# Performance work log

Hardware: AMD Instinct MI355X
Metric: run time of the kernel (lower is better)

Reference implementation:

```python
import jax, jax.numpy as jnp
import numpy as np

TEMP = 0.05
MOMENTUM = 0.2
EPS = 1e-12
B, D, N = 256, 2048, 30000


def setup_inputs() -> dict:
    key = jax.random.key(0)
    k1, k2, k3 = jax.random.split(key, 3)
    inputs = jax.random.normal(k1, (B, D), dtype=jnp.float32)
    feats = jax.random.normal(k2, (N, D), dtype=jnp.float32)
    # cluster memory bank rows are unit-normalized in practice
    feats = feats / (jnp.linalg.norm(feats, axis=1, keepdims=True) + EPS)
    targets = jax.random.randint(k3, (B,), 0, N, dtype=jnp.int64)
    return {"inputs": inputs, "features": feats, "targets": targets}


def reference(inputs, features, targets):
    # F.normalize(inputs, dim=1)
    x = inputs / (jnp.linalg.norm(inputs, axis=1, keepdims=True) + EPS)
    # outputs = x @ features.T / temp  -> [B, N]
    logits = jnp.einsum("bd,nd->bn", x, features) / TEMP
    # loss = F.cross_entropy(outputs, targets)
    logp = jax.nn.log_softmax(logits, axis=1)
    loss = -jnp.mean(jnp.take_along_axis(logp, targets[:, None], axis=1))

    # CM backward side effect: sequential per-sample momentum update + renorm of bank.
    # features[y] = m*features[y] + (1-m)*x ; features[y] /= ||features[y]||
    def step(bank, xy):
        xi, yi = xy
        f = MOMENTUM * bank[yi] + (1.0 - MOMENTUM) * xi
        f = f / (jnp.linalg.norm(f) + EPS)
        return bank.at[yi].set(f), None

    new_features, _ = jax.lax.scan(step, features, (x, targets))
    return loss, new_features
```

## Files before the change

kernel.cpp:

```cpp
#include <hip/hip_runtime.h>
#include <hip/hip_bf16.h>

#define B_ 256
#define D_ 2048
#define N_ 30000
#define INV_TEMP 20.0f
#define MOM 0.2f
#define EPSF 1e-12f
#define BN 48
#define KC 64
#define KH 1024
#define NKH 16
#define NT 625
#define NBL 40
#define TPB 16

typedef __attribute__((ext_vector_type(8))) short bf16x8;
typedef __attribute__((ext_vector_type(4))) float f32x4;

typedef const __attribute__((address_space(1))) void* gas_t;
typedef __attribute__((address_space(3))) void* las_t;
#define GLOAD16(g, l) __builtin_amdgcn_global_load_lds((gas_t)(g), (las_t)(l), 16, 0, 0)

__device__ __forceinline__ unsigned short f2bf(float f) {
  union { float f; unsigned int u; } v; v.f = f;
  unsigned int u = v.u;
  unsigned int r = (u + 0x7fffu + ((u >> 16) & 1u)) >> 16;
  return (unsigned short)r;
}

__device__ __forceinline__ float blockReduceSum256(float v) {
  __shared__ float red[4];
  #pragma unroll
  for (int m = 32; m >= 1; m >>= 1) v += __shfl_xor(v, m, 64);
  int lane = threadIdx.x & 63, w = threadIdx.x >> 6;
  __syncthreads();
  if (lane == 0) red[w] = v;
  __syncthreads();
  return red[0] + red[1] + red[2] + red[3];
}

__global__ __launch_bounds__(256) void knorm(const float* __restrict__ in,
                                             float* __restrict__ x,
                                             unsigned short* __restrict__ xbf) {
  int b = blockIdx.x, t = threadIdx.x;
  const float* row = in + (size_t)b * D_;
  float vals[8]; float ss = 0.f;
  #pragma unroll
  for (int i = 0; i < 8; i++) { float f = row[t + i * 256]; vals[i] = f; ss += f * f; }
  float tot = blockReduceSum256(ss);
  float inv = 1.0f / (sqrtf(tot) + EPSF);
  #pragma unroll
  for (int i = 0; i < 8; i++) {
    float xv = vals[i] * inv;
    x[(size_t)b * D_ + t + i * 256] = xv;
    xbf[(size_t)b * D_ + t + i * 256] = f2bf(xv);
  }
}

__global__ __launch_bounds__(256, 4) void kmain(const float* __restrict__ feats,
                                                const unsigned short* __restrict__ xbf,
                                                float* __restrict__ outp,
                                                float* __restrict__ pacc) {
  __shared__ __align__(16) unsigned short xs[16384];
  __shared__ __align__(16) unsigned short fs[3072];
  int tid = threadIdx.x, wave = tid >> 6, lane = tid & 63;
  int nb = blockIdx.x >> 1, kh = blockIdx.x & 1;
  int n0 = nb * BN, kbase = kh * KH;
  int q = lane >> 4, lr = lane & 15;
  int slp = (lane & 48) | ((lane - 1) & 15);
  int slc = (lane & 48) | 15;

  int gswz = (lane & 7) ^ (lane >> 3);
  int rof = wave * 8 + (lane >> 3);
  const char* xsrc = (const char*)xbf;

  int fn[3], fc[3];
  #pragma unroll
  for (int i = 0; i < 3; i++) { int fi = tid + i * 256; fn[i] = fi >> 4; fc[i] = fi & 15; }
  float carry[3] = {0.f, 0.f, 0.f};

  f32x4 acc[4][3];
  #pragma unroll
  for (int i = 0; i < 4; i++)
    #pragma unroll
    for (int j = 0; j < 3; j++) acc[i][j] = f32x4{0.f, 0.f, 0.f, 0.f};

  for (int t = 0; t < NKH; t++) {
    int k0 = kbase + t * KC;
    __syncthreads();
    float4 fv[3];
    #pragma unroll
    for (int i = 0; i < 3; i++)
      fv[i] = *(const float4*)(feats + (size_t)(n0 + fn[i]) * D_ + k0 + 4 * fc[i]);
    size_t gb = ((size_t)rof * D_ + k0 + gswz * 8) * 2;
    #pragma unroll
    for (int i = 0; i < 8; i++)
      GLOAD16(xsrc + gb + (size_t)i * 32 * D_ * 2,
              (char*)xs + i * 4096 + wave * 1024);
    #pragma unroll
    for (int i = 0; i < 3; i++) {
      float4 v = fv[i];
      union { __hip_bfloat162 h2[2]; uint2 u8; } pk;
      pk.h2[0] = __float22bfloat162_rn(make_float2(v.x, v.y));
      pk.h2[1] = __float22bfloat162_rn(make_float2(v.z, v.w));
      int byte = fn[i] * 128 + ((8 * fc[i]) ^ ((fn[i] & 7) << 4));
      *(uint2*)((char*)fs + byte) = pk.u8;
      float pw_p = __shfl(v.w, slp, 64);
      float pw_c = __shfl(carry[i], slc, 64);
      float prev = (fc[i] == 0) ? pw_c : pw_p;
      size_t rb = (size_t)(n0 + fn[i]) * D_ + k0 + 4 * fc[i];
      if (t == 0 && fc[i] == 0) {
        outp[rb + 1] = v.x; outp[rb + 2] = v.y; outp[rb + 3] = v.z;
      } else {
        *(float4*)(outp + rb) = make_float4(prev, v.x, v.y, v.z);
      }
      carry[i] = v.w;
    }
    __syncthreads();
    #pragma unroll
    for (int ks = 0; ks < 2; ks++) {
      int g = ks * 4 + q;
      bf16x8 a[4], bb[3];
      #pragma unroll
      for (int mi = 0; mi < 4; mi++) {
        int row = wave * 64 + mi * 16 + lr;
        a[mi] = *(const bf16x8*)((char*)xs + row * 128 + ((g * 16) ^ ((row & 7) << 4)));
      }
      #pragma unroll
      for (int ni = 0; ni < 3; ni++) {
        int row = ni * 16 + lr;
        bb[ni] = *(const bf16x8*)((char*)fs + row * 128 + ((g * 16) ^ ((row & 7) << 4)));
      }
      #pragma unroll
      for (int mi = 0; mi < 4; mi++)
        #pragma unroll
        for (int ni = 0; ni < 3; ni++)
          acc[mi][ni] = __builtin_amdgcn_mfma_f32_16x16x32_bf16(a[mi], bb[ni], acc[mi][ni], 0, 0, 0);
    }
  }

  #pragma unroll
  for (int i = 0; i < 3; i++)
    if (fc[i] == 15)
      outp[(size_t)(n0 + fn[i]) * D_ + kbase + KH] = carry[i];

  float* pb = pacc + (size_t)blockIdx.x * (256 * 48);
  #pragma unroll
  for (int mi = 0; mi < 4; mi++)
    #pragma unroll
    for (int r = 0; r < 4; r++) {
      int row = wave * 64 + mi * 16 + q * 4 + r;
      #pragma unroll
      for (int ni = 0; ni < 3; ni++)
        pb[row * 48 + ni * 16 + lr] = acc[mi][ni][r];
    }
}

__global__ __launch_bounds__(256) void kacc(const float* __restrict__ pacc,
                                            float* __restrict__ pmax,
                                            float* __restrict__ psum) {
  int nb = blockIdx.x, b = threadIdx.x;
  const float* p0 = pacc + ((size_t)2 * nb) * (256 * 48) + b * 48;
  const float* p1 = p0 + 256 * 48;
  float v[48];
  float mx = -INFINITY;
  #pragma unroll
  for (int c = 0; c < 48; c += 4) {
    float4 a = *(const float4*)(p0 + c);
    float4 d = *(const float4*)(p1 + c);
    v[c + 0] = (a.x + d.x) * INV_TEMP;
    v[c + 1] = (a.y + d.y) * INV_TEMP;
    v[c + 2] = (a.z + d.z) * INV_TEMP;
    v[c + 3] = (a.w + d.w) * INV_TEMP;
    mx = fmaxf(mx, fmaxf(fmaxf(v[c], v[c + 1]), fmaxf(v[c + 2], v[c + 3])));
  }
  float s = 0.f;
  #pragma unroll
  for (int c = 0; c < 48; c++) s += __expf(v[c] - mx);
  pmax[(size_t)nb * 256 + b] = mx;
  psum[(size_t)nb * 256 + b] = s;
}

__global__ __launch_bounds__(256) void ktdot(const float* __restrict__ feats,
                                             const float* __restrict__ x,
                                             const int* __restrict__ tgt,
                                             float* __restrict__ tdot) {
  int b = blockIdx.x, t = threadIdx.x;
  int y = tgt[b];
  const float* fr = feats + (size_t)y * D_;
  const float* xr = x + (size_t)b * D_;
  float s = 0.f;
  #pragma unroll
  for (int i = 0; i < 8; i++) s += fr[t + i * 256] * xr[t + i * 256];
  float tot = blockReduceSum256(s);
  if (t == 0) tdot[b] = tot * INV_TEMP;
}

__global__ __launch_bounds__(256) void kloss1(const float* __restrict__ pmax,
                                              const float* __restrict__ psum,
                                              float* __restrict__ pm2,
                                              float* __restrict__ ps2) {
  int b = threadIdx.x, j = blockIdx.x;
  float m = -INFINITY, s = 0.f;
  #pragma unroll 4
  for (int i = 0; i < TPB; i++) {
    int tile = j * TPB + i;
    if (tile >= NT) break;
    float mt = pmax[(size_t)tile * 256 + b];
    float st = psum[(size_t)tile * 256 + b];
    if (mt > m) { s = s * __expf(m - mt) + st; m = mt; }
    else        { s += st * __expf(mt - m); }
  }
  pm2[j * 256 + b] = m;
  ps2[j * 256 + b] = s;
}

__global__ __launch_bounds__(256) void kloss2(const float* __restrict__ pm2,
                                              const float* __restrict__ ps2,
                                              const float* __restrict__ tdot,
                                              float* __restrict__ out) {
  int b = threadIdx.x;
  float m = -INFINITY, s = 0.f;
  for (int j = 0; j < NBL; j++) {
    float mt = pm2[j * 256 + b];
    float st = ps2[j * 256 + b];
    float M = fmaxf(m, mt);
    s = s * __expf(m - M) + st * __expf(mt - M);
    m = M;
  }
  float lb = m + logf(s) - tdot[b];
  float tot = blockReduceSum256(lb);
  if (b == 0) out[0] = tot * (1.0f / 256.0f);
}

__global__ __launch_bounds__(256) void kupdate(const float* __restrict__ feats,
                                               const float* __restrict__ x,
                                               const int* __restrict__ tgt,
                                               float* __restrict__ outF) {
  int b = blockIdx.x, t = threadIdx.x;
  int y = tgt[b];
  for (int i = 0; i < b; i++) if (tgt[i] == y) return;
  float f[8];
  #pragma unroll
  for (int i = 0; i < 8; i++) f[i] = feats[(size_t)y * D_ + t + i * 256];
  for (int b2 = b; b2 < B_; b2++) {
    if (tgt[b2] != y) continue;
    float ss = 0.f;
    #pragma unroll
    for (int i = 0; i < 8; i++) {
      f[i] = MOM * f[i] + (1.0f - MOM) * x[(size_t)b2 * D_ + t + i * 256];
      ss += f[i] * f[i];
    }
    float tot = blockReduceSum256(ss);
    float inv = 1.0f / (sqrtf(tot) + EPSF);
    #pragma unroll
    for (int i = 0; i < 8; i++) f[i] *= inv;
  }
  #pragma unroll
  for (int i = 0; i < 8; i++) outF[(size_t)y * D_ + t + i * 256] = f[i];
}

extern "C" void kernel_launch(void* const* d_in, const int* in_sizes, int n_in,
                              void* d_out, int out_size, void* d_ws, size_t ws_size,
                              hipStream_t stream) {
  const float* inputs = (const float*)d_in[0];
  const float* feats  = (const float*)d_in[1];
  const int*   tgt    = (const int*)d_in[2];
  float* out  = (float*)d_out;
  float* outF = out + 1;

  char* ws = (char*)d_ws;
  float*          pacc = (float*)ws;
  size_t off = (size_t)1250 * 256 * 48 * 4;
  float*          x    = (float*)(ws + off);            off += (size_t)B_ * D_ * 4;
  unsigned short* xbf  = (unsigned short*)(ws + off);   off += (size_t)B_ * D_ * 2;
  float*          pmax = (float*)(ws + off);            off += (size_t)NT * 256 * 4;
  float*          psum = (float*)(ws + off);            off += (size_t)NT * 256 * 4;
  float*          pm2  = (float*)(ws + off);            off += (size_t)NBL * 256 * 4;
  float*          ps2  = (float*)(ws + off);            off += (size_t)NBL * 256 * 4;
  float*          tdot = (float*)(ws + off);

  hipLaunchKernelGGL(knorm,   dim3(B_),    dim3(256), 0, stream, inputs, x, xbf);
  hipLaunchKernelGGL(kmain,   dim3(1250),  dim3(256), 0, stream, feats, xbf, out, pacc);
  hipLaunchKernelGGL(kacc,    dim3(NT),    dim3(256), 0, stream, pacc, pmax, psum);
  hipLaunchKernelGGL(ktdot,   dim3(B_),    dim3(256), 0, stream, feats, x, tgt, tdot);
  hipLaunchKernelGGL(kloss1,  dim3(NBL),   dim3(256), 0, stream, pmax, psum, pm2, ps2);
  hipLaunchKernelGGL(kloss2,  dim3(1),     dim3(256), 0, stream, pm2, ps2, tdot, out);
  hipLaunchKernelGGL(kupdate, dim3(B_),    dim3(256), 0, stream, feats, x, tgt, outF);
}
```

Before: 222.1 us.

## Split GEMM over batch halves with fused softmax partials, separate bank copy

The main GEMM now splits the batch (M) dimension across block pairs instead of the K dimension, so each block covers the full K range and computes the per-row max and sum-exp for its 48-column tile in registers via shuffles. This removes the large partial-accumulator buffer and the separate kacc kernel. The memory-bank copy to the output, previously fused into the GEMM's feature loads, moves to a standalone grid-stride kernel. The cost is reading the feature bank twice (once in the GEMM, once in the copy) and running a longer K loop per block.

```diff
diff --git a/kernel.cpp b/kernel.cpp
--- a/kernel.cpp
+++ b/kernel.cpp
@@ -7,11 +7,11 @@
 #define INV_TEMP 20.0f
 #define MOM 0.2f
 #define EPSF 1e-12f
+#define BM 128
 #define BN 48
 #define KC 64
-#define KH 1024
-#define NKH 16
 #define NT 625
+#define NK 32
 #define NBL 40
 #define TPB 16
 
@@ -58,36 +58,33 @@
   }
 }
 
-__global__ __launch_bounds__(256, 4) void kmain(const float* __restrict__ feats,
+__global__ __launch_bounds__(256, 6) void kmain(const float* __restrict__ feats,
                                                 const unsigned short* __restrict__ xbf,
-                                                float* __restrict__ outp,
-                                                float* __restrict__ pacc) {
-  __shared__ __align__(16) unsigned short xs[16384];
+                                                float* __restrict__ pmax,
+                                                float* __restrict__ psum) {
+  __shared__ __align__(16) unsigned short xs[8192];
   __shared__ __align__(16) unsigned short fs[3072];
   int tid = threadIdx.x, wave = tid >> 6, lane = tid & 63;
-  int nb = blockIdx.x >> 1, kh = blockIdx.x & 1;
-  int n0 = nb * BN, kbase = kh * KH;
+  int nb = blockIdx.x >> 1, mb = blockIdx.x & 1;
+  int n0 = nb * BN;
   int q = lane >> 4, lr = lane & 15;
-  int slp = (lane & 48) | ((lane - 1) & 15);
-  int slc = (lane & 48) | 15;
 
   int gswz = (lane & 7) ^ (lane >> 3);
-  int rof = wave * 8 + (lane >> 3);
+  int rof = mb * BM + wave * 8 + (lane >> 3);
   const char* xsrc = (const char*)xbf;
 
   int fn[3], fc[3];
   #pragma unroll
   for (int i = 0; i < 3; i++) { int fi = tid + i * 256; fn[i] = fi >> 4; fc[i] = fi & 15; }
-  float carry[3] = {0.f, 0.f, 0.f};
-
-  f32x4 acc[4][3];
-  #pragma unroll
-  for (int i = 0; i < 4; i++)
+
+  f32x4 acc[2][3];
+  #pragma unroll
+  for (int i = 0; i < 2; i++)
     #pragma unroll
     for (int j = 0; j < 3; j++) acc[i][j] = f32x4{0.f, 0.f, 0.f, 0.f};
 
-  for (int t = 0; t < NKH; t++) {
-    int k0 = kbase + t * KC;
+  for (int t = 0; t < NK; t++) {
+    int k0 = t * KC;
     __syncthreads();
     float4 fv[3];
     #pragma unroll
@@ -95,36 +92,25 @@
       fv[i] = *(const float4*)(feats + (size_t)(n0 + fn[i]) * D_ + k0 + 4 * fc[i]);
     size_t gb = ((size_t)rof * D_ + k0 + gswz * 8) * 2;
     #pragma unroll
-    for (int i = 0; i < 8; i++)
+    for (int i = 0; i < 4; i++)
       GLOAD16(xsrc + gb + (size_t)i * 32 * D_ * 2,
               (char*)xs + i * 4096 + wave * 1024);
     #pragma unroll
     for (int i = 0; i < 3; i++) {
-      float4 v = fv[i];
       union { __hip_bfloat162 h2[2]; uint2 u8; } pk;
-      pk.h2[0] = __float22bfloat162_rn(make_float2(v.x, v.y));
-      pk.h2[1] = __float22bfloat162_rn(make_float2(v.z, v.w));
+      pk.h2[0] = __float22bfloat162_rn(make_float2(fv[i].x, fv[i].y));
+      pk.h2[1] = __float22bfloat162_rn(make_float2(fv[i].z, fv[i].w));
       int byte = fn[i] * 128 + ((8 * fc[i]) ^ ((fn[i] & 7) << 4));
       *(uint2*)((char*)fs + byte) = pk.u8;
-      float pw_p = __shfl(v.w, slp, 64);
-      float pw_c = __shfl(carry[i], slc, 64);
-      float prev = (fc[i] == 0) ? pw_c : pw_p;
-      size_t rb = (size_t)(n0 + fn[i]) * D_ + k0 + 4 * fc[i];
-      if (t == 0 && fc[i] == 0) {
-        outp[rb + 1] = v.x; outp[rb + 2] = v.y; outp[rb + 3] = v.z;
-      } else {
-        *(float4*)(outp + rb) = make_float4(prev, v.x, v.y, v.z);
-      }
-      carry[i] = v.w;
     }
     __syncthreads();
     #pragma unroll
     for (int ks = 0; ks < 2; ks++) {
       int g = ks * 4 + q;
-      bf16x8 a[4], bb[3];
-      #pragma unroll
-      for (int mi = 0; mi < 4; mi++) {
-        int row = wave * 64 + mi * 16 + lr;
+      bf16x8 a[2], bb[3];
+      #pragma unroll
+      for (int mi = 0; mi < 2; mi++) {
+        int row = wave * 32 + mi * 16 + lr;
         a[mi] = *(const bf16x8*)((char*)xs + row * 128 + ((g * 16) ^ ((row & 7) << 4)));
       }
       #pragma unroll
@@ -133,7 +119,7 @@
         bb[ni] = *(const bf16x8*)((char*)fs + row * 128 + ((g * 16) ^ ((row & 7) << 4)));
       }
       #pragma unroll
-      for (int mi = 0; mi < 4; mi++)
+      for (int mi = 0; mi < 2; mi++)
         #pragma unroll
         for (int ni = 0; ni < 3; ni++)
           acc[mi][ni] = __builtin_amdgcn_mfma_f32_16x16x32_bf16(a[mi], bb[ni], acc[mi][ni], 0, 0, 0);
@@ -141,45 +127,41 @@
   }
 
   #pragma unroll
-  for (int i = 0; i < 3; i++)
-    if (fc[i] == 15)
-      outp[(size_t)(n0 + fn[i]) * D_ + kbase + KH] = carry[i];
-
-  float* pb = pacc + (size_t)blockIdx.x * (256 * 48);
-  #pragma unroll
-  for (int mi = 0; mi < 4; mi++)
+  for (int mi = 0; mi < 2; mi++) {
     #pragma unroll
     for (int r = 0; r < 4; r++) {
-      int row = wave * 64 + mi * 16 + q * 4 + r;
-      #pragma unroll
-      for (int ni = 0; ni < 3; ni++)
-        pb[row * 48 + ni * 16 + lr] = acc[mi][ni][r];
-    }
-}
-
-__global__ __launch_bounds__(256) void kacc(const float* __restrict__ pacc,
-                                            float* __restrict__ pmax,
-                                            float* __restrict__ psum) {
-  int nb = blockIdx.x, b = threadIdx.x;
-  const float* p0 = pacc + ((size_t)2 * nb) * (256 * 48) + b * 48;
-  const float* p1 = p0 + 256 * 48;
-  float v[48];
-  float mx = -INFINITY;
-  #pragma unroll
-  for (int c = 0; c < 48; c += 4) {
-    float4 a = *(const float4*)(p0 + c);
-    float4 d = *(const float4*)(p1 + c);
-    v[c + 0] = (a.x + d.x) * INV_TEMP;
-    v[c + 1] = (a.y + d.y) * INV_TEMP;
-    v[c + 2] = (a.z + d.z) * INV_TEMP;
-    v[c + 3] = (a.w + d.w) * INV_TEMP;
-    mx = fmaxf(mx, fmaxf(fmaxf(v[c], v[c + 1]), fmaxf(v[c + 2], v[c + 3])));
-  }
-  float s = 0.f;
-  #pragma unroll
-  for (int c = 0; c < 48; c++) s += __expf(v[c] - mx);
-  pmax[(size_t)nb * 256 + b] = mx;
-  psum[(size_t)nb * 256 + b] = s;
+      float v0 = acc[mi][0][r] * INV_TEMP;
+      float v1 = acc[mi][1][r] * INV_TEMP;
+      float v2 = acc[mi][2][r] * INV_TEMP;
+      float mx = fmaxf(fmaxf(v0, v1), v2);
+      #pragma unroll
+      for (int m = 8; m >= 1; m >>= 1) mx = fmaxf(mx, __shfl_xor(mx, m, 64));
+      float s = __expf(v0 - mx) + __expf(v1 - mx) + __expf(v2 - mx);
+      #pragma unroll
+      for (int m = 8; m >= 1; m >>= 1) s += __shfl_xor(s, m, 64);
+      if (lr == 0) {
+        int row = mb * BM + wave * 32 + mi * 16 + q * 4 + r;
+        pmax[(size_t)nb * 256 + row] = mx;
+        psum[(size_t)nb * 256 + row] = s;
+      }
+    }
+  }
+}
+
+__global__ __launch_bounds__(256) void kcopy(const float* __restrict__ feats,
+                                             float* __restrict__ outp) {
+  const size_t NF4 = (size_t)N_ * D_ / 4;
+  size_t stride = (size_t)gridDim.x * 256;
+  int lane = threadIdx.x & 63;
+  int slp = (lane - 1) & 63;
+  for (size_t idx = (size_t)blockIdx.x * 256 + threadIdx.x; idx < NF4; idx += stride) {
+    float4 v = *(const float4*)(feats + 4 * idx);
+    float pw = __shfl(v.w, slp, 64);
+    float prev = (lane == 0) ? ((idx == 0) ? 0.f : feats[4 * idx - 1]) : pw;
+    if (idx == 0) { outp[1] = v.x; outp[2] = v.y; outp[3] = v.z; }
+    else *(float4*)(outp + 4 * idx) = make_float4(prev, v.x, v.y, v.z);
+    if (idx == NF4 - 1) outp[4 * idx + 4] = v.w;
+  }
 }
 
 __global__ __launch_bounds__(256) void ktdot(const float* __restrict__ feats,
@@ -271,8 +253,7 @@
   float* outF = out + 1;
 
   char* ws = (char*)d_ws;
-  float*          pacc = (float*)ws;
-  size_t off = (size_t)1250 * 256 * 48 * 4;
+  size_t off = 0;
   float*          x    = (float*)(ws + off);            off += (size_t)B_ * D_ * 4;
   unsigned short* xbf  = (unsigned short*)(ws + off);   off += (size_t)B_ * D_ * 2;
   float*          pmax = (float*)(ws + off);            off += (size_t)NT * 256 * 4;
@@ -282,10 +263,10 @@
   float*          tdot = (float*)(ws + off);
 
   hipLaunchKernelGGL(knorm,   dim3(B_),    dim3(256), 0, stream, inputs, x, xbf);
-  hipLaunchKernelGGL(kmain,   dim3(1250),  dim3(256), 0, stream, feats, xbf, out, pacc);
-  hipLaunchKernelGGL(kacc,    dim3(NT),    dim3(256), 0, stream, pacc, pmax, psum);
+  hipLaunchKernelGGL(kmain,   dim3(1250),  dim3(256), 0, stream, feats, xbf, pmax, psum);
   hipLaunchKernelGGL(ktdot,   dim3(B_),    dim3(256), 0, stream, feats, x, tgt, tdot);
   hipLaunchKernelGGL(kloss1,  dim3(NBL),   dim3(256), 0, stream, pmax, psum, pm2, ps2);
   hipLaunchKernelGGL(kloss2,  dim3(1),     dim3(256), 0, stream, pm2, ps2, tdot, out);
+  hipLaunchKernelGGL(kcopy,   dim3(2048),  dim3(256), 0, stream, feats, out);
   hipLaunchKernelGGL(kupdate, dim3(B_),    dim3(256), 0, stream, feats, x, tgt, outF);
 }
```

Measured after the change: 216.9 us. 2.3% less time.
